# Kernel optimization log

Hardware: AMD Instinct MI355X
Metric: run time of the kernel (lower is better)

## Reference

```python
import jax, jax.numpy as jnp
import numpy as np

WINDOW = 25  # causal sliding-window size for trend extraction


def setup_inputs() -> dict:
    key = jax.random.key(0)
    kx, kw1, kb1, kw2, kb2 = jax.random.split(key, 5)
    T = 720
    bound = 1.0 / np.sqrt(T)
    x = jax.random.normal(kx, (32, 512, T), dtype=jnp.float32)
    trend_w = jax.random.uniform(kw1, (T, T), jnp.float32, -bound, bound)
    trend_b = jax.random.uniform(kb1, (T,), jnp.float32, -bound, bound)
    seasonal_w = jax.random.uniform(kw2, (T, T), jnp.float32, -bound, bound)
    seasonal_b = jax.random.uniform(kb2, (T,), jnp.float32, -bound, bound)
    return {"x": x, "trend_w": trend_w, "trend_b": trend_b,
            "seasonal_w": seasonal_w, "seasonal_b": seasonal_b}


def _causal_window_mean(x, window):
    # x: [B, N, T]; trend[..., j] = mean(x[..., max(0, j-window+1):j+1])
    T = x.shape[-1]
    cs = jnp.cumsum(x, axis=-1)
    cs_shift = jnp.concatenate(
        [jnp.zeros(x.shape[:-1] + (window,), x.dtype), cs[..., :T - window]], axis=-1)
    counts = jnp.minimum(jnp.arange(T) + 1, window).astype(x.dtype)
    return (cs - cs_shift) / counts


def reference(x, trend_w, trend_b, seasonal_w, seasonal_b):
    trend = _causal_window_mean(x, WINDOW)
    seasonal = x - trend
    trend_out = jnp.einsum('bnt,ut->bnu', trend, trend_w) + trend_b
    seasonal_out = jnp.einsum('bnt,ut->bnu', seasonal, seasonal_w) + seasonal_b
    return trend_out + seasonal_out
```

## Files before the change

kernel.cpp:

```cpp
#include <hip/hip_runtime.h>
#include <hip/hip_bf16.h>


#define Tdim  720
#define KP    736
#define WROWS 768
#define NK    23
#define BM    64
#define APAD  744

using bf16x8 = __attribute__((ext_vector_type(8))) __bf16;
using f32x4  = __attribute__((ext_vector_type(4))) float;

__global__ void fold_w_kernel(const float* __restrict__ tw,
                              const float* __restrict__ tb,
                              const float* __restrict__ sw,
                              const float* __restrict__ sb,
                              __bf16* __restrict__ Wb,
                              float* __restrict__ beff) {
  int idx = blockIdx.x * 256 + threadIdx.x;
  if (idx >= WROWS * KP) return;
  int u = idx / KP;
  int i = idx - u * KP;
  float w = 0.0f;
  if (u < Tdim && i < Tdim) {
    const float* twr = tw + (size_t)u * Tdim;
    const float* swr = sw + (size_t)u * Tdim;
    int tend = (i + 25 < Tdim) ? (i + 25) : Tdim;
    float acc = 0.0f;
    if (i >= 24) {
      #pragma unroll 5
      for (int t = i; t < tend; ++t) acc += twr[t] - swr[t];
      acc *= 0.04f;
    } else {
      for (int t = i; t < tend; ++t) {
        float c = (t >= 24) ? 0.04f : 1.0f / (float)(t + 1);
        acc += (twr[t] - swr[t]) * c;
      }
    }
    w = swr[i] + acc;
  }
  Wb[idx] = (__bf16)w;
  if (i == 0 && u < Tdim) beff[u] = tb[u] + sb[u];
}

__global__ __launch_bounds__(1024, 1)
void dlinear_gemm(const float* __restrict__ x,
                  const __bf16* __restrict__ Wb,
                  const float* __restrict__ beff,
                  float* __restrict__ out) {
  __shared__ __bf16 As[BM * APAD];

  const int tid  = threadIdx.x;
  const int lane = tid & 63;
  const int wid  = tid >> 6;
  const int lg = lane >> 4, lr = lane & 15;

  const int m0 = blockIdx.x * BM;
  const int u0 = wid * 48;

  #pragma unroll
  for (int c = 0; c < 6; ++c) {
    int idx = tid + 1024 * c;
    if (idx < BM * 90) {
      int row  = idx / 90;
      int col8 = idx - row * 90;
      const float* p = x + (size_t)(m0 + row) * Tdim + col8 * 8;
      f32x4 a0 = ((const f32x4*)p)[0];
      f32x4 a1 = ((const f32x4*)p)[1];
      bf16x8 v;
      #pragma unroll
      for (int j = 0; j < 4; ++j) { v[j] = (__bf16)a0[j]; v[j + 4] = (__bf16)a1[j]; }
      *(bf16x8*)(&As[row * APAD + col8 * 8]) = v;
    }
  }
  {
    int r = tid >> 4;
    int c = 720 + (tid & 15);
    As[r * APAD + c] = (__bf16)0.0f;
  }
  __syncthreads();

  const __bf16* wp[3];
  #pragma unroll
  for (int ni = 0; ni < 3; ++ni)
    wp[ni] = Wb + (size_t)(u0 + ni * 16 + lr) * KP + lg * 8;

  int arofs[4];
  #pragma unroll
  for (int mi = 0; mi < 4; ++mi) arofs[mi] = (mi * 16 + lr) * APAD + lg * 8;

  f32x4 acc[4][3];
  #pragma unroll
  for (int mi = 0; mi < 4; ++mi)
    #pragma unroll
    for (int ni = 0; ni < 3; ++ni) {
      f32x4 z; z[0] = 0.f; z[1] = 0.f; z[2] = 0.f; z[3] = 0.f;
      acc[mi][ni] = z;
    }

  bf16x8 b0[3], b1[3];
  #pragma unroll
  for (int ni = 0; ni < 3; ++ni) b0[ni] = *(const bf16x8*)wp[ni];

  for (int t = 0; t < NK - 1; t += 2) {
    #pragma unroll
    for (int ni = 0; ni < 3; ++ni) b1[ni] = *(const bf16x8*)(wp[ni] + (t + 1) * 32);
    {
      bf16x8 av[4];
      #pragma unroll
      for (int mi = 0; mi < 4; ++mi) av[mi] = *(const bf16x8*)(&As[arofs[mi] + t * 32]);
      #pragma unroll
      for (int mi = 0; mi < 4; ++mi)
        #pragma unroll
        for (int ni = 0; ni < 3; ++ni)
          acc[mi][ni] = __builtin_amdgcn_mfma_f32_16x16x32_bf16(av[mi], b0[ni],
                                                                acc[mi][ni], 0, 0, 0);
    }
    #pragma unroll
    for (int ni = 0; ni < 3; ++ni) b0[ni] = *(const bf16x8*)(wp[ni] + (t + 2) * 32);
    {
      bf16x8 av[4];
      #pragma unroll
      for (int mi = 0; mi < 4; ++mi) av[mi] = *(const bf16x8*)(&As[arofs[mi] + (t + 1) * 32]);
      #pragma unroll
      for (int mi = 0; mi < 4; ++mi)
        #pragma unroll
        for (int ni = 0; ni < 3; ++ni)
          acc[mi][ni] = __builtin_amdgcn_mfma_f32_16x16x32_bf16(av[mi], b1[ni],
                                                                acc[mi][ni], 0, 0, 0);
    }
  }
  {
    bf16x8 av[4];
    #pragma unroll
    for (int mi = 0; mi < 4; ++mi) av[mi] = *(const bf16x8*)(&As[arofs[mi] + 22 * 32]);
    #pragma unroll
    for (int mi = 0; mi < 4; ++mi)
      #pragma unroll
      for (int ni = 0; ni < 3; ++ni)
        acc[mi][ni] = __builtin_amdgcn_mfma_f32_16x16x32_bf16(av[mi], b0[ni],
                                                              acc[mi][ni], 0, 0, 0);
  }

  #pragma unroll
  for (int ni = 0; ni < 3; ++ni) {
    const int u = u0 + ni * 16 + lr;
    if (u >= Tdim) continue;
    const float bias = beff[u];
    #pragma unroll
    for (int mi = 0; mi < 4; ++mi) {
      const int mb = m0 + mi * 16 + lg * 4;
      #pragma unroll
      for (int j = 0; j < 4; ++j)
        out[(size_t)(mb + j) * Tdim + u] = acc[mi][ni][j] + bias;
    }
  }
}

extern "C" void kernel_launch(void* const* d_in, const int* in_sizes, int n_in,
                              void* d_out, int out_size, void* d_ws, size_t ws_size,
                              hipStream_t stream) {
  const float* x  = (const float*)d_in[0];
  const float* tw = (const float*)d_in[1];
  const float* tb = (const float*)d_in[2];
  const float* sw = (const float*)d_in[3];
  const float* sb = (const float*)d_in[4];
  float* out = (float*)d_out;

  __bf16* Wb  = (__bf16*)d_ws;
  float* beff = (float*)((char*)d_ws + (size_t)WROWS * KP * sizeof(__bf16));

  const int fold_total = WROWS * KP;
  fold_w_kernel<<<dim3((fold_total + 255) / 256), dim3(256), 0, stream>>>(
      tw, tb, sw, sb, Wb, beff);

  const int M = in_sizes[0] / Tdim;
  dim3 grid(M / BM);
  dlinear_gemm<<<grid, dim3(1024), 0, stream>>>(x, Wb, beff, out);
}
```

Measured before the change: 49.08 us.

## Stage x tile loading in three K chunks overlapped with MFMA compute

The x tile is now loaded and converted in three K-chunks (columns 0-255, 256-511, 512-735) instead of all at once before compute. The global loads for the next chunk are issued before the MFMA loop over the current chunk and written to LDS afterwards, so load latency is hidden behind matrix math. The zero padding for columns 720-735 moves into the last chunk. It costs two extra block barriers and more registers held across the loops, which matters at 1024 threads per block.

```diff
diff --git a/kernel.cpp b/kernel.cpp
--- a/kernel.cpp
+++ b/kernel.cpp
@@ -59,28 +59,6 @@
   const int m0 = blockIdx.x * BM;
   const int u0 = wid * 48;
 
-  #pragma unroll
-  for (int c = 0; c < 6; ++c) {
-    int idx = tid + 1024 * c;
-    if (idx < BM * 90) {
-      int row  = idx / 90;
-      int col8 = idx - row * 90;
-      const float* p = x + (size_t)(m0 + row) * Tdim + col8 * 8;
-      f32x4 a0 = ((const f32x4*)p)[0];
-      f32x4 a1 = ((const f32x4*)p)[1];
-      bf16x8 v;
-      #pragma unroll
-      for (int j = 0; j < 4; ++j) { v[j] = (__bf16)a0[j]; v[j + 4] = (__bf16)a1[j]; }
-      *(bf16x8*)(&As[row * APAD + col8 * 8]) = v;
-    }
-  }
-  {
-    int r = tid >> 4;
-    int c = 720 + (tid & 15);
-    As[r * APAD + c] = (__bf16)0.0f;
-  }
-  __syncthreads();
-
   const __bf16* wp[3];
   #pragma unroll
   for (int ni = 0; ni < 3; ++ni)
@@ -99,47 +77,122 @@
       acc[mi][ni] = z;
     }
 
-  bf16x8 b0[3], b1[3];
-  #pragma unroll
-  for (int ni = 0; ni < 3; ++ni) b0[ni] = *(const bf16x8*)wp[ni];
-
-  for (int t = 0; t < NK - 1; t += 2) {
-    #pragma unroll
-    for (int ni = 0; ni < 3; ++ni) b1[ni] = *(const bf16x8*)(wp[ni] + (t + 1) * 32);
-    {
-      bf16x8 av[4];
-      #pragma unroll
-      for (int mi = 0; mi < 4; ++mi) av[mi] = *(const bf16x8*)(&As[arofs[mi] + t * 32]);
-      #pragma unroll
-      for (int mi = 0; mi < 4; ++mi)
-        #pragma unroll
-        for (int ni = 0; ni < 3; ++ni)
-          acc[mi][ni] = __builtin_amdgcn_mfma_f32_16x16x32_bf16(av[mi], b0[ni],
-                                                                acc[mi][ni], 0, 0, 0);
-    }
-    #pragma unroll
-    for (int ni = 0; ni < 3; ++ni) b0[ni] = *(const bf16x8*)(wp[ni] + (t + 2) * 32);
-    {
-      bf16x8 av[4];
-      #pragma unroll
-      for (int mi = 0; mi < 4; ++mi) av[mi] = *(const bf16x8*)(&As[arofs[mi] + (t + 1) * 32]);
-      #pragma unroll
-      for (int mi = 0; mi < 4; ++mi)
-        #pragma unroll
-        for (int ni = 0; ni < 3; ++ni)
-          acc[mi][ni] = __builtin_amdgcn_mfma_f32_16x16x32_bf16(av[mi], b1[ni],
-                                                                acc[mi][ni], 0, 0, 0);
-    }
-  }
-  {
+  bf16x8 bb[2][3];
+  #pragma unroll
+  for (int ni = 0; ni < 3; ++ni) bb[0][ni] = *(const bf16x8*)wp[ni];
+
+  {
+    const int unit0 = tid, unit1 = tid + 1024;
+    const float* p0 = x + (size_t)(m0 + (unit0 >> 5)) * Tdim + (unit0 & 31) * 8;
+    const float* p1 = x + (size_t)(m0 + (unit1 >> 5)) * Tdim + (unit1 & 31) * 8;
+    f32x4 a0 = ((const f32x4*)p0)[0], a1 = ((const f32x4*)p0)[1];
+    f32x4 a2 = ((const f32x4*)p1)[0], a3 = ((const f32x4*)p1)[1];
+    bf16x8 v0, v1;
+    #pragma unroll
+    for (int j = 0; j < 4; ++j) {
+      v0[j] = (__bf16)a0[j]; v0[j + 4] = (__bf16)a1[j];
+      v1[j] = (__bf16)a2[j]; v1[j + 4] = (__bf16)a3[j];
+    }
+    *(bf16x8*)(&As[(unit0 >> 5) * APAD + (unit0 & 31) * 8]) = v0;
+    *(bf16x8*)(&As[(unit1 >> 5) * APAD + (unit1 & 31) * 8]) = v1;
+  }
+  __syncthreads();
+
+  f32x4 c1a0, c1a1, c1b0, c1b1;
+  {
+    const int unit0 = tid, unit1 = tid + 1024;
+    const float* p0 = x + (size_t)(m0 + (unit0 >> 5)) * Tdim + 256 + (unit0 & 31) * 8;
+    const float* p1 = x + (size_t)(m0 + (unit1 >> 5)) * Tdim + 256 + (unit1 & 31) * 8;
+    c1a0 = ((const f32x4*)p0)[0]; c1a1 = ((const f32x4*)p0)[1];
+    c1b0 = ((const f32x4*)p1)[0]; c1b1 = ((const f32x4*)p1)[1];
+  }
+  #pragma unroll
+  for (int t = 0; t < 8; ++t) {
+    #pragma unroll
+    for (int ni = 0; ni < 3; ++ni)
+      bb[(t + 1) & 1][ni] = *(const bf16x8*)(wp[ni] + (t + 1) * 32);
     bf16x8 av[4];
     #pragma unroll
-    for (int mi = 0; mi < 4; ++mi) av[mi] = *(const bf16x8*)(&As[arofs[mi] + 22 * 32]);
+    for (int mi = 0; mi < 4; ++mi) av[mi] = *(const bf16x8*)(&As[arofs[mi] + t * 32]);
     #pragma unroll
     for (int mi = 0; mi < 4; ++mi)
       #pragma unroll
       for (int ni = 0; ni < 3; ++ni)
-        acc[mi][ni] = __builtin_amdgcn_mfma_f32_16x16x32_bf16(av[mi], b0[ni],
+        acc[mi][ni] = __builtin_amdgcn_mfma_f32_16x16x32_bf16(av[mi], bb[t & 1][ni],
+                                                              acc[mi][ni], 0, 0, 0);
+  }
+  {
+    const int unit0 = tid, unit1 = tid + 1024;
+    bf16x8 v0, v1;
+    #pragma unroll
+    for (int j = 0; j < 4; ++j) {
+      v0[j] = (__bf16)c1a0[j]; v0[j + 4] = (__bf16)c1a1[j];
+      v1[j] = (__bf16)c1b0[j]; v1[j + 4] = (__bf16)c1b1[j];
+    }
+    *(bf16x8*)(&As[(unit0 >> 5) * APAD + 256 + (unit0 & 31) * 8]) = v0;
+    *(bf16x8*)(&As[(unit1 >> 5) * APAD + 256 + (unit1 & 31) * 8]) = v1;
+  }
+  __syncthreads();
+
+  f32x4 c2a0, c2a1, c2b0, c2b1;
+  const int u2_0 = tid, u2_1 = tid + 1024;
+  const int r20 = u2_0 / 28, c20 = u2_0 - r20 * 28;
+  const int r21 = u2_1 / 28, c21 = u2_1 - r21 * 28;
+  const bool v20 = (c20 < 26);
+  const bool v21 = (u2_1 < 1792) && (c21 < 26);
+  if (v20) {
+    const float* p = x + (size_t)(m0 + r20) * Tdim + 512 + c20 * 8;
+    c2a0 = ((const f32x4*)p)[0]; c2a1 = ((const f32x4*)p)[1];
+  }
+  if (v21) {
+    const float* p = x + (size_t)(m0 + r21) * Tdim + 512 + c21 * 8;
+    c2b0 = ((const f32x4*)p)[0]; c2b1 = ((const f32x4*)p)[1];
+  }
+  #pragma unroll
+  for (int t = 8; t < 16; ++t) {
+    #pragma unroll
+    for (int ni = 0; ni < 3; ++ni)
+      bb[(t + 1) & 1][ni] = *(const bf16x8*)(wp[ni] + (t + 1) * 32);
+    bf16x8 av[4];
+    #pragma unroll
+    for (int mi = 0; mi < 4; ++mi) av[mi] = *(const bf16x8*)(&As[arofs[mi] + t * 32]);
+    #pragma unroll
+    for (int mi = 0; mi < 4; ++mi)
+      #pragma unroll
+      for (int ni = 0; ni < 3; ++ni)
+        acc[mi][ni] = __builtin_amdgcn_mfma_f32_16x16x32_bf16(av[mi], bb[t & 1][ni],
+                                                              acc[mi][ni], 0, 0, 0);
+  }
+  {
+    bf16x8 v0, v1;
+    #pragma unroll
+    for (int j = 0; j < 4; ++j) {
+      v0[j] = v20 ? (__bf16)c2a0[j] : (__bf16)0.0f;
+      v0[j + 4] = v20 ? (__bf16)c2a1[j] : (__bf16)0.0f;
+      v1[j] = v21 ? (__bf16)c2b0[j] : (__bf16)0.0f;
+      v1[j + 4] = v21 ? (__bf16)c2b1[j] : (__bf16)0.0f;
+    }
+    *(bf16x8*)(&As[r20 * APAD + 512 + c20 * 8]) = v0;
+    if (u2_1 < 1792)
+      *(bf16x8*)(&As[r21 * APAD + 512 + c21 * 8]) = v1;
+  }
+  __syncthreads();
+
+  #pragma unroll
+  for (int t = 16; t < 23; ++t) {
+    if (t < 22) {
+      #pragma unroll
+      for (int ni = 0; ni < 3; ++ni)
+        bb[(t + 1) & 1][ni] = *(const bf16x8*)(wp[ni] + (t + 1) * 32);
+    }
+    bf16x8 av[4];
+    #pragma unroll
+    for (int mi = 0; mi < 4; ++mi) av[mi] = *(const bf16x8*)(&As[arofs[mi] + t * 32]);
+    #pragma unroll
+    for (int mi = 0; mi < 4; ++mi)
+      #pragma unroll
+      for (int ni = 0; ni < 3; ++ni)
+        acc[mi][ni] = __builtin_amdgcn_mfma_f32_16x16x32_bf16(av[mi], bb[t & 1][ni],
                                                               acc[mi][ni], 0, 0, 0);
   }
 
```

Measured after the change: 53.52 us. 1.09x slower.
